# Performance work log

Measured on AMD Instinct MI355X. Metric: run time of the kernel, lower is better.

Reference implementation:

```python
import jax, jax.numpy as jnp
import numpy as np

D = 768      # input_dim
O = 768      # output_dim
E = 8        # num_experts
H = 10 * D   # expert hidden dim (fixed by module: input_dim * 10)
N = 4096     # tokens


def setup_inputs() -> dict:
    key = jax.random.key(0)
    ks = jax.random.split(key, 7)
    s = lambda fan_in: 1.0 / np.sqrt(fan_in)
    x  = jax.random.normal(ks[0], (N, D), dtype=jnp.float32)
    Wg = jax.random.uniform(ks[1], (D, E), jnp.float32, -s(D), s(D))
    bg = jax.random.uniform(ks[2], (E,),   jnp.float32, -s(D), s(D))
    W1 = jax.random.uniform(ks[3], (E, D, H), jnp.float32, -s(D), s(D))
    b1 = jax.random.uniform(ks[4], (E, H),    jnp.float32, -s(D), s(D))
    W2 = jax.random.uniform(ks[5], (E, H, O), jnp.float32, -s(H), s(H))
    b2 = jax.random.uniform(ks[6], (E, O),    jnp.float32, -s(H), s(H))
    return {"x": x, "Wg": Wg, "bg": bg, "W1": W1, "b1": b1, "W2": W2, "b2": b2}


def reference(x, Wg, bg, W1, b1, W2, b2):
    # gating: softmax over experts, keep only top-1 prob (rest zeroed)
    gate_probs = jax.nn.softmax(x @ Wg + bg, axis=1)          # [N, E]
    top_vals, top_idx = jax.lax.top_k(gate_probs, 1)           # [N, 1]
    gate_masked = jnp.zeros_like(gate_probs).at[
        jnp.arange(x.shape[0]), top_idx[:, 0]].set(top_vals[:, 0])
    # dense all-experts MLP (module computes every expert for every token)
    h = jax.nn.relu(jnp.einsum('nd,edh->neh', x, W1) + b1)     # [N, E, H]
    expert_out = jnp.einsum('neh,eho->neo', h, W2) + b2        # [N, E, O]
    # bmm combine: [N,1,E] @ [N,E,O] -> [N,O]
    return jnp.einsum('ne,neo->no', gate_masked, expert_out)
```

## Files before the change

kernel.cpp:

```cpp
#include <hip/hip_runtime.h>
#include <hip/hip_bf16.h>
#include <stdint.h>

#define N_TOK 4096
#define DIM   768
#define NE    8
#define HDIM  7680
#define ODIM  768
#define MAXTILES 40

typedef __bf16 bf16x8 __attribute__((ext_vector_type(8)));
typedef float f32x4 __attribute__((ext_vector_type(4)));

__device__ __forceinline__ unsigned short f2bf(float f) {
    union { float f; unsigned u; } v; v.f = f;
    return (unsigned short)((v.u + 0x7fffu + ((v.u >> 16) & 1u)) >> 16);
}

__device__ __forceinline__ unsigned cvt_pk_bf16(float lo, float hi) {
    unsigned r;
    asm("v_cvt_pk_bf16_f32 %0, %1, %2" : "=v"(r) : "v"(lo), "v"(hi));
    return r;
}

__device__ __forceinline__ void gload_lds16(const unsigned short* g, unsigned short* l) {
    __builtin_amdgcn_global_load_lds(
        (const __attribute__((address_space(1))) unsigned int*)g,
        (__attribute__((address_space(3))) unsigned int*)l, 16, 0, 0);
}

__global__ void moe_gating(const float* __restrict__ x, const float* __restrict__ Wg,
                           const float* __restrict__ bg, int* __restrict__ cnt,
                           int* __restrict__ top_e, int* __restrict__ rnk,
                           float* __restrict__ top_p) {
    const int wid  = threadIdx.x >> 6;
    const int lane = threadIdx.x & 63;
    const int t = blockIdx.x * 4 + wid;
    double p[NE];
#pragma unroll
    for (int j = 0; j < NE; ++j) p[j] = 0.0;
    const float* xr  = x  + (size_t)t * DIM + lane * 12;
    const float* wr0 = Wg + lane * 12 * NE;
#pragma unroll
    for (int i = 0; i < 12; ++i) {
        double xv = (double)xr[i];
#pragma unroll
        for (int j = 0; j < NE; ++j) p[j] += xv * (double)wr0[i * NE + j];
    }
#pragma unroll
    for (int off = 32; off >= 1; off >>= 1)
#pragma unroll
        for (int j = 0; j < NE; ++j) p[j] += __shfl_xor(p[j], off, 64);
    if (lane == 0) {
        double l[NE];
#pragma unroll
        for (int j = 0; j < NE; ++j) l[j] = p[j] + (double)bg[j];
        int be = 0; double bl = l[0];
#pragma unroll
        for (int j = 1; j < NE; ++j) if (l[j] > bl) { bl = l[j]; be = j; }
        double s = 0.0;
#pragma unroll
        for (int j = 0; j < NE; ++j) s += exp(l[j] - bl);
        int rk = atomicAdd(&cnt[be], 1);
        top_e[t] = be; rnk[t] = rk; top_p[t] = (float)(1.0 / s);
    }
}

__global__ void moe_init(int* cnt) { if (threadIdx.x < NE) cnt[threadIdx.x] = 0; }

__global__ void moe_scan(const int* __restrict__ cnt, int* __restrict__ offs,
                         int* __restrict__ tbl, int* __restrict__ ntt) {
    if (threadIdx.x == 0) {
        int s = 0, nt = 0;
        for (int e = 0; e < NE; ++e) {
            offs[e] = s;
            int m = (cnt[e] + 127) >> 7;
            for (int i = 0; i < m; ++i) tbl[nt++] = (e << 8) | i;
            s += cnt[e];
        }
        ntt[0] = nt;
    }
}

__global__ void moe_mkperm(const int* __restrict__ top_e, const int* __restrict__ rnk,
                           const float* __restrict__ top_p, const int* __restrict__ offs,
                           int* __restrict__ perm, float* __restrict__ gate_s) {
    int t = blockIdx.x * 256 + threadIdx.x;
    int e = top_e[t];
    int slot = offs[e] + rnk[t];
    perm[slot] = t;
    gate_s[slot] = top_p[t];
}

__global__ void moe_gather(const float* __restrict__ x, const int* __restrict__ perm,
                           unsigned short* __restrict__ Xg) {
    int slot = blockIdx.x;
    int t = perm[slot];
    const float* src = x + (size_t)t * DIM;
    unsigned short* dst = Xg + (size_t)slot * DIM;
    for (int i = threadIdx.x; i < DIM; i += 256) dst[i] = f2bf(src[i]);
}

__global__ void moe_initout(const int* __restrict__ top_e, const float* __restrict__ top_p,
                            const float* __restrict__ b2, float* __restrict__ out) {
    int t = blockIdx.x;
    int e = top_e[t];
    float gv = top_p[t];
    const float* b = b2 + (size_t)e * ODIM;
    float* o = out + (size_t)t * ODIM;
    for (int i = threadIdx.x; i < ODIM; i += 256) o[i] = gv * b[i];
}

template<int LAYER>
__global__ __launch_bounds__(256, 3) void moe_gemm(
    const unsigned short* __restrict__ A, const float* __restrict__ B,
    const float* __restrict__ bias, const int* __restrict__ cnt,
    const int* __restrict__ offs, const int* __restrict__ perm,
    const float* __restrict__ gate_s, const int* __restrict__ tbl,
    const int* __restrict__ ntt, unsigned short* __restrict__ H,
    float* __restrict__ out) {

    constexpr int NT    = (LAYER == 1) ? HDIM : ODIM;
    constexpr int AST   = (LAYER == 1) ? DIM  : HDIM;
    constexpr int KFULL = (LAYER == 1) ? DIM  : HDIM;
    constexpr int KBLK  = (LAYER == 1) ? DIM  : HDIM / 4;
    constexpr int NITER = KBLK / 32;

    const int ent = blockIdx.x;
    if (ent >= ntt[0]) return;
    const int tt = tbl[ent];
    const int e  = tt >> 8;
    const int mt = tt & 255;
    const int ks = (LAYER == 1) ? 0 : blockIdx.z;
    const int ne = cnt[e];
    const int base = offs[e];
    const int n0 = blockIdx.y * 128;
    const int mlim = ne - mt * 128;
    const int kbase = ks * KBLK;

    __shared__ unsigned short As[2][4096];
    __shared__ unsigned short Bs[2][4096];

    const int tid = threadIdx.x;
    const int lane = tid & 63, w = tid >> 6;
    const int wr = w >> 1, wc = w & 1;
    const int g = lane >> 4, r = lane & 15;

    const int rl0 = 2 * w * 16 + r;
    const int rl1 = rl0 + 16;
    const int cr0 = rl0 < mlim ? rl0 : mlim - 1;
    const int cr1 = rl1 < mlim ? rl1 : mlim - 1;
    const unsigned short* aS0 = A + (size_t)(base + mt * 128 + cr0) * AST + kbase + g * 8;
    const unsigned short* aS1 = A + (size_t)(base + mt * 128 + cr1) * AST + kbase + g * 8;
    const int aD0 = (2 * w) * 512;
    const int aD1 = aD0 + 512;

    const int bn = tid & 127;
    const int kh = tid >> 7;
    const float* bS = B + (size_t)e * KFULL * NT + (size_t)(kbase + kh * 16) * NT + n0 + bn;
    const int bD = (bn >> 4) * 512 + (kh * 2) * 128 + (bn & 15) * 8;

    f32x4 acc[4][4] = {};
    float bvA[16], bvB[16];

#define FENCE __builtin_amdgcn_sched_barrier(0)

#define LOADB(dst_, t_)                                                        \
    do { const float* bp_ = bS + (size_t)((t_) * 32) * NT;                     \
        _Pragma("unroll")                                                      \
        for (int i_ = 0; i_ < 16; ++i_) dst_[i_] = bp_[(size_t)i_ * NT];       \
    } while (0)

#define DMA_A(t_, buf_)                                                        \
    do { gload_lds16(aS0 + (t_) * 32, &As[buf_][aD0]);                         \
         gload_lds16(aS1 + (t_) * 32, &As[buf_][aD1]); } while (0)

#define COMMITB(src_, buf_)                                                    \
    do { uint4 q0_, q1_;                                                       \
        q0_.x = cvt_pk_bf16(src_[0],  src_[1]);  q0_.y = cvt_pk_bf16(src_[2],  src_[3]);  \
        q0_.z = cvt_pk_bf16(src_[4],  src_[5]);  q0_.w = cvt_pk_bf16(src_[6],  src_[7]);  \
        q1_.x = cvt_pk_bf16(src_[8],  src_[9]);  q1_.y = cvt_pk_bf16(src_[10], src_[11]); \
        q1_.z = cvt_pk_bf16(src_[12], src_[13]); q1_.w = cvt_pk_bf16(src_[14], src_[15]); \
        *(uint4*)&Bs[buf_][bD]       = q0_;                                    \
        *(uint4*)&Bs[buf_][bD + 128] = q1_;                                    \
    } while (0)

#define BODY(t_, cur_, LDst_, CMsrc_, MODE_)                                   \
    do {                                                                       \
        bf16x8 af_[4], bf_[4];                                                 \
        _Pragma("unroll")                                                      \
        for (int m_ = 0; m_ < 4; ++m_)                                         \
            af_[m_] = *(const bf16x8*)&As[cur_][(wr * 4 + m_) * 512 + lane * 8]; \
        _Pragma("unroll")                                                      \
        for (int n_ = 0; n_ < 4; ++n_)                                         \
            bf_[n_] = *(const bf16x8*)&Bs[cur_][(wc * 4 + n_) * 512 + lane * 8]; \
        FENCE;                                                                 \
        if (MODE_ >= 1) DMA_A((t_) + 1, (cur_) ^ 1);                           \
        FENCE;                                                                 \
        if (MODE_ == 2) LOADB(LDst_, (t_) + 2);                                \
        asm volatile("s_waitcnt lgkmcnt(0)" ::: "memory");                     \
        FENCE;                                                                 \
        _Pragma("unroll")                                                      \
        for (int n_ = 0; n_ < 4; ++n_)                                         \
            _Pragma("unroll")                                                  \
            for (int m_ = 0; m_ < 4; ++m_)                                     \
                acc[m_][n_] = __builtin_amdgcn_mfma_f32_16x16x32_bf16(         \
                    af_[m_], bf_[n_], acc[m_][n_], 0, 0, 0);                   \
        FENCE;                                                                 \
        if (MODE_ == 2) { asm volatile("s_waitcnt vmcnt(16)" ::: "memory"); }  \
        else if (MODE_ == 1) { asm volatile("s_waitcnt vmcnt(0)" ::: "memory"); } \
        if (MODE_ >= 1) {                                                      \
            COMMITB(CMsrc_, (cur_) ^ 1);                                       \
            asm volatile("s_waitcnt lgkmcnt(0)" ::: "memory");                 \
            __builtin_amdgcn_s_barrier();                                      \
            FENCE;                                                             \
        }                                                                      \
    } while (0)

    LOADB(bvA, 0);
    FENCE;
    DMA_A(0, 0);
    FENCE;
    LOADB(bvB, 1);
    asm volatile("s_waitcnt vmcnt(16)" ::: "memory");
    FENCE;
    COMMITB(bvA, 0);
    asm volatile("s_waitcnt lgkmcnt(0)" ::: "memory");
    __builtin_amdgcn_s_barrier();
    FENCE;

#pragma unroll 1
    for (int t = 0; t + 4 <= NITER; t += 2) {
        BODY(t,     0, bvA, bvB, 2);
        BODY(t + 1, 1, bvB, bvA, 2);
    }
    BODY(NITER - 2, 0, bvA, bvB, 1);
    BODY(NITER - 1, 1, bvB, bvA, 0);

#undef BODY
#undef COMMITB
#undef DMA_A
#undef LOADB
#undef FENCE

#pragma unroll
    for (int m = 0; m < 4; ++m) {
#pragma unroll
        for (int j = 0; j < 4; ++j) {
            int lrow = mt * 128 + wr * 64 + m * 16 + g * 4 + j;
            if (lrow < ne) {
                int slot = base + lrow;
#pragma unroll
                for (int n = 0; n < 4; ++n) {
                    int col = n0 + wc * 64 + n * 16 + r;
                    if constexpr (LAYER == 1) {
                        float v = acc[m][n][j] + bias[(size_t)e * NT + col];
                        v = fmaxf(v, 0.0f);
                        H[(size_t)slot * HDIM + col] = f2bf(v);
                    } else {
                        atomicAdd(&out[(size_t)perm[slot] * ODIM + col],
                                  gate_s[slot] * acc[m][n][j]);
                    }
                }
            }
        }
    }
}

extern "C" void kernel_launch(void* const* d_in, const int* in_sizes, int n_in,
                              void* d_out, int out_size, void* d_ws, size_t ws_size,
                              hipStream_t stream) {
    const float* x  = (const float*)d_in[0];
    const float* Wg = (const float*)d_in[1];
    const float* bg = (const float*)d_in[2];
    const float* W1 = (const float*)d_in[3];
    const float* b1 = (const float*)d_in[4];
    const float* W2 = (const float*)d_in[5];
    const float* b2 = (const float*)d_in[6];
    float* out = (float*)d_out;

    char* ws = (char*)d_ws;
    int*   cnt    = (int*)(ws + 0);
    int*   offs   = (int*)(ws + 64);
    int*   ntt    = (int*)(ws + 96);
    int*   tbl    = (int*)(ws + 128);
    int*   top_e  = (int*)(ws + 1024);
    int*   rnk    = (int*)(ws + 1024 + 16384);
    float* top_p  = (float*)(ws + 1024 + 2 * 16384);
    int*   perm   = (int*)(ws + 1024 + 3 * 16384);
    float* gate_s = (float*)(ws + 1024 + 4 * 16384);
    unsigned short* Xg = (unsigned short*)(ws + 82944);
    unsigned short* H  = (unsigned short*)(ws + 82944 + (size_t)N_TOK * DIM * 2);

    moe_init<<<1, 64, 0, stream>>>(cnt);
    moe_gating<<<N_TOK / 4, 256, 0, stream>>>(x, Wg, bg, cnt, top_e, rnk, top_p);
    moe_scan<<<1, 64, 0, stream>>>(cnt, offs, tbl, ntt);
    moe_mkperm<<<N_TOK / 256, 256, 0, stream>>>(top_e, rnk, top_p, offs, perm, gate_s);
    moe_gather<<<N_TOK, 256, 0, stream>>>(x, perm, Xg);
    moe_initout<<<N_TOK, 256, 0, stream>>>(top_e, top_p, b2, out);

    moe_gemm<1><<<dim3(MAXTILES, HDIM / 128, 1), 256, 0, stream>>>(
        Xg, W1, b1, cnt, offs, perm, gate_s, tbl, ntt, H, out);
    moe_gemm<2><<<dim3(MAXTILES, ODIM / 128, 4), 256, 0, stream>>>(
        H, W2, b2, cnt, offs, perm, gate_s, tbl, ntt, H, out);
}
```

Before: 409.2 us.

## Flatten GEMM grids into tile tables ordered for weight reuse across CUs

Replaces the 3D grid (m-tile x n-tile x k-split), which had many early-exit blocks, with a flat 1D grid whose block-to-tile mapping comes from precomputed tables. A new scan and fill stage spreads (expert, n-tile, k-split) columns across eight lanes, so consecutive blocks share the same expert weight columns, and marks unused slots with -1. The goal is better L2 reuse of the fp32 weights and fewer idle blocks. It also raises the launch-bounds occupancy hint from 3 to 4, which may add register pressure or spills, and it adds one more small kernel launch.

```diff
diff --git a/kernel.cpp b/kernel.cpp
--- a/kernel.cpp
+++ b/kernel.cpp
@@ -7,7 +7,8 @@
 #define NE    8
 #define HDIM  7680
 #define ODIM  768
-#define MAXTILES 40
+#define G1GRID 2816
+#define G2GRID 1280
 
 typedef __bf16 bf16x8 __attribute__((ext_vector_type(8)));
 typedef float f32x4 __attribute__((ext_vector_type(4)));
@@ -69,16 +70,40 @@
 __global__ void moe_init(int* cnt) { if (threadIdx.x < NE) cnt[threadIdx.x] = 0; }
 
 __global__ void moe_scan(const int* __restrict__ cnt, int* __restrict__ offs,
-                         int* __restrict__ tbl, int* __restrict__ ntt) {
-    if (threadIdx.x == 0) {
-        int s = 0, nt = 0;
-        for (int e = 0; e < NE; ++e) {
-            offs[e] = s;
-            int m = (cnt[e] + 127) >> 7;
-            for (int i = 0; i < m; ++i) tbl[nt++] = (e << 8) | i;
-            s += cnt[e];
-        }
-        ntt[0] = nt;
+                         int* __restrict__ mc, int* __restrict__ g1s,
+                         int* __restrict__ g2s) {
+    __shared__ int smc[NE];
+    int tid = threadIdx.x;
+    if (tid == 0) { int s = 0; for (int e = 0; e < NE; ++e) { offs[e] = s; s += cnt[e]; } }
+    if (tid < NE) { smc[tid] = (cnt[tid] + 127) >> 7; mc[tid] = smc[tid]; }
+    __syncthreads();
+    if (tid < 8) {
+        int s = 0;
+        for (int j = 0; j < 60; ++j) { int p = tid + 8 * j; g1s[p] = s; s += smc[p / 60]; }
+        int s2 = 0;
+        for (int j = 0; j < 24; ++j) { int p = tid + 8 * j; g2s[p] = s2; s2 += smc[p / 24]; }
+    }
+}
+
+__global__ void moe_fill(const int* __restrict__ mc, const int* __restrict__ g1s,
+                         const int* __restrict__ g2s, int* __restrict__ tbl1,
+                         int* __restrict__ tbl2) {
+    int gid = blockIdx.x * 256 + threadIdx.x;
+    if (gid < G1GRID) {
+        int c = gid & 7, slot = gid >> 3;
+        int sel = c;
+        for (int j = 0; j < 60; ++j) { int p = c + 8 * j; if (g1s[p] <= slot) sel = p; else break; }
+        int e = sel / 60, n0 = sel % 60;
+        int mt = slot - g1s[sel];
+        tbl1[gid] = (mt < mc[e]) ? ((e << 14) | (mt << 8) | (n0 << 2)) : -1;
+    } else if (gid < G1GRID + G2GRID) {
+        int gg = gid - G1GRID;
+        int c = gg & 7, slot = gg >> 3;
+        int sel = c;
+        for (int j = 0; j < 24; ++j) { int p = c + 8 * j; if (g2s[p] <= slot) sel = p; else break; }
+        int e = sel / 24, q = sel % 24;
+        int mt = slot - g2s[sel];
+        tbl2[gg] = (mt < mc[e]) ? ((e << 14) | (mt << 8) | ((q >> 2) << 2) | (q & 3)) : -1;
     }
 }
 
@@ -112,13 +137,12 @@
 }
 
 template<int LAYER>
-__global__ __launch_bounds__(256, 3) void moe_gemm(
+__global__ __launch_bounds__(256, 4) void moe_gemm(
     const unsigned short* __restrict__ A, const float* __restrict__ B,
     const float* __restrict__ bias, const int* __restrict__ cnt,
     const int* __restrict__ offs, const int* __restrict__ perm,
     const float* __restrict__ gate_s, const int* __restrict__ tbl,
-    const int* __restrict__ ntt, unsigned short* __restrict__ H,
-    float* __restrict__ out) {
+    unsigned short* __restrict__ H, float* __restrict__ out) {
 
     constexpr int NT    = (LAYER == 1) ? HDIM : ODIM;
     constexpr int AST   = (LAYER == 1) ? DIM  : HDIM;
@@ -126,15 +150,14 @@
     constexpr int KBLK  = (LAYER == 1) ? DIM  : HDIM / 4;
     constexpr int NITER = KBLK / 32;
 
-    const int ent = blockIdx.x;
-    if (ent >= ntt[0]) return;
-    const int tt = tbl[ent];
-    const int e  = tt >> 8;
-    const int mt = tt & 255;
-    const int ks = (LAYER == 1) ? 0 : blockIdx.z;
+    const int code = tbl[blockIdx.x];
+    if (code < 0) return;
+    const int e  = code >> 14;
+    const int mt = (code >> 8) & 63;
+    const int n0 = ((code >> 2) & 63) * 128;
+    const int ks = code & 3;
     const int ne = cnt[e];
     const int base = offs[e];
-    const int n0 = blockIdx.y * 128;
     const int mlim = ne - mt * 128;
     const int kbase = ks * KBLK;
 
@@ -282,25 +305,27 @@
     char* ws = (char*)d_ws;
     int*   cnt    = (int*)(ws + 0);
     int*   offs   = (int*)(ws + 64);
-    int*   ntt    = (int*)(ws + 96);
-    int*   tbl    = (int*)(ws + 128);
-    int*   top_e  = (int*)(ws + 1024);
-    int*   rnk    = (int*)(ws + 1024 + 16384);
-    float* top_p  = (float*)(ws + 1024 + 2 * 16384);
-    int*   perm   = (int*)(ws + 1024 + 3 * 16384);
-    float* gate_s = (float*)(ws + 1024 + 4 * 16384);
-    unsigned short* Xg = (unsigned short*)(ws + 82944);
-    unsigned short* H  = (unsigned short*)(ws + 82944 + (size_t)N_TOK * DIM * 2);
+    int*   mc     = (int*)(ws + 128);
+    int*   g1s    = (int*)(ws + 256);
+    int*   g2s    = (int*)(ws + 2304);
+    int*   tbl1   = (int*)(ws + 3072);
+    int*   tbl2   = (int*)(ws + 14336);
+    int*   top_e  = (int*)(ws + 19456);
+    int*   rnk    = (int*)(ws + 19456 + 16384);
+    float* top_p  = (float*)(ws + 19456 + 2 * 16384);
+    int*   perm   = (int*)(ws + 19456 + 3 * 16384);
+    float* gate_s = (float*)(ws + 19456 + 4 * 16384);
+    unsigned short* Xg = (unsigned short*)(ws + 101376);
+    unsigned short* H  = (unsigned short*)(ws + 101376 + (size_t)N_TOK * DIM * 2);
 
     moe_init<<<1, 64, 0, stream>>>(cnt);
     moe_gating<<<N_TOK / 4, 256, 0, stream>>>(x, Wg, bg, cnt, top_e, rnk, top_p);
-    moe_scan<<<1, 64, 0, stream>>>(cnt, offs, tbl, ntt);
+    moe_scan<<<1, 64, 0, stream>>>(cnt, offs, mc, g1s, g2s);
+    moe_fill<<<(G1GRID + G2GRID) / 256, 256, 0, stream>>>(mc, g1s, g2s, tbl1, tbl2);
     moe_mkperm<<<N_TOK / 256, 256, 0, stream>>>(top_e, rnk, top_p, offs, perm, gate_s);
     moe_gather<<<N_TOK, 256, 0, stream>>>(x, perm, Xg);
     moe_initout<<<N_TOK, 256, 0, stream>>>(top_e, top_p, b2, out);
 
-    moe_gemm<1><<<dim3(MAXTILES, HDIM / 128, 1), 256, 0, stream>>>(
-        Xg, W1, b1, cnt, offs, perm, gate_s, tbl, ntt, H, out);
-    moe_gemm<2><<<dim3(MAXTILES, ODIM / 128, 4), 256, 0, stream>>>(
-        H, W2, b2, cnt, offs, perm, gate_s, tbl, ntt, H, out);
-}
+    moe_gemm<1><<<G1GRID, 256, 0, stream>>>(Xg, W1, b1, cnt, offs, perm, gate_s, tbl1, H, out);
+    moe_gemm<2><<<G2GRID, 256, 0, stream>>>(H, W2, b2, cnt, offs, perm, gate_s, tbl2, H, out);
+}
```

After: 1.048 ms. 156% more time.
